# Optimization experiments

Hardware: AMD Instinct MI355X
Metric: run time of the kernel (lower is better)

The kernel has to match this reference:

```python
import jax, jax.numpy as jnp
import numpy as np


def setup_inputs() -> dict:
    key = jax.random.key(0)
    ks = jax.random.split(key, 7)
    B, N, D, F, E = 4, 2048, 1024, 4096, 8
    s_in = 1.0 / np.sqrt(D)
    s_ff = 1.0 / np.sqrt(F)
    return {
        "x": jax.random.normal(ks[0], (B, N, D), dtype=jnp.float32),
        "Wg": jax.random.normal(ks[1], (D, E), dtype=jnp.float32) * s_in,
        "bg": jnp.zeros((E,), dtype=jnp.float32),
        "W1": jax.random.normal(ks[2], (E, D, F), dtype=jnp.float32) * s_in,
        "b1": jnp.zeros((E, F), dtype=jnp.float32),
        "W2": jax.random.normal(ks[3], (E, F, D), dtype=jnp.float32) * s_ff,
        "b2": jnp.zeros((E, D), dtype=jnp.float32),
    }


def reference(x, Wg, bg, W1, b1, W2, b2):
    TOP_K = 2
    # Gating: softmax over experts, then top-k (dropout is inference no-op)
    gate_scores = jax.nn.softmax(x @ Wg + bg, axis=-1)          # [B,N,E]
    topk_scores, topk_idx = jax.lax.top_k(gate_scores, TOP_K)   # [B,N,K]

    # Dense all-expert FFN (matches reference: every expert on every token)
    h = jax.nn.relu(jnp.einsum("bnd,edf->ebnf", x, W1) + b1[:, None, None, :])
    eo = jnp.einsum("ebnf,efd->ebnd", h, W2) + b2[:, None, None, :]  # [E,B,N,D]

    # Gather top-k expert outputs per token and combine
    eo_bne = jnp.transpose(eo, (1, 2, 0, 3))                     # [B,N,E,D]
    gathered = jnp.take_along_axis(eo_bne, topk_idx[..., None], axis=2)  # [B,N,K,D]
    output = jnp.sum(topk_scores[..., None] * gathered, axis=2)  # [B,N,D]
    return output
```

## Files before the change

kernel.cpp:

```cpp
#include <hip/hip_runtime.h>
#include <stdint.h>


#define E_ 8
#define D_ 1024
#define F_ 4096
#define NTOK 8192

typedef __bf16 bf16x8 __attribute__((ext_vector_type(8)));
typedef float f32x4 __attribute__((ext_vector_type(4)));
typedef unsigned short ushort_t;

__device__ __forceinline__ ushort_t f2bf(float f) {
  union { float f; unsigned u; } v; v.f = f;
  unsigned r = v.u + 0x7fff + ((v.u >> 16) & 1);
  return (ushort_t)(r >> 16);
}

__device__ __forceinline__ void gload16(const void* g, void* l) {
  __builtin_amdgcn_global_load_lds((__attribute__((address_space(1))) void*)(g),
                                   (__attribute__((address_space(3))) void*)(l),
                                   16, 0, 0);
}

__global__ __launch_bounds__(256) void gate_k(const float* __restrict__ x,
    const float* __restrict__ Wg, const float* __restrict__ bg,
    int* counts, int* tk_idx, float* tk_score) {
  __shared__ float wg[D_ * E_];
  for (int i = threadIdx.x; i < D_ * E_; i += 256) wg[i] = Wg[i];
  __syncthreads();
  const int lane = threadIdx.x & 63;
  const int wv = threadIdx.x >> 6;
  const int t = blockIdx.x * 4 + wv;
  const float* xr = x + (size_t)t * D_;
  double acc[E_];
#pragma unroll
  for (int e = 0; e < E_; ++e) acc[e] = 0.0;
  for (int i = 0; i < D_ / 64; ++i) {
    const int d = i * 64 + lane;
    const double xv = (double)xr[d];
#pragma unroll
    for (int e = 0; e < E_; ++e) acc[e] += xv * (double)wg[d * E_ + e];
  }
#pragma unroll
  for (int e = 0; e < E_; ++e) {
    double v = acc[e];
#pragma unroll
    for (int s = 32; s > 0; s >>= 1) v += __shfl_xor(v, s, 64);
    acc[e] = v;
  }
  if (lane == 0) {
    double l[E_], m = -1e300;
#pragma unroll
    for (int e = 0; e < E_; ++e) { l[e] = acc[e] + (double)bg[e]; m = (l[e] > m) ? l[e] : m; }
    double p[E_], s = 0.0;
#pragma unroll
    for (int e = 0; e < E_; ++e) { p[e] = exp(l[e] - m); s += p[e]; }
    int i1 = 0;
#pragma unroll
    for (int e = 1; e < E_; ++e) if (p[e] > p[i1]) i1 = e;
    int i2 = -1;
#pragma unroll
    for (int e = 0; e < E_; ++e) if (e != i1 && (i2 < 0 || p[e] > p[i2])) i2 = e;
    tk_idx[2 * t] = i1; tk_idx[2 * t + 1] = i2;
    tk_score[2 * t] = (float)(p[i1] / s);
    tk_score[2 * t + 1] = (float)(p[i2] / s);
    atomicAdd(&counts[i1], 1);
    atomicAdd(&counts[i2], 1);
  }
}

__global__ void offsets_k(const int* __restrict__ counts, int* __restrict__ offsets) {
  if (threadIdx.x == 0) {
    int s = 0;
    for (int e = 0; e < E_; ++e) { offsets[e] = s; s += counts[e]; }
    offsets[E_] = s;
  }
}

__global__ __launch_bounds__(256) void assign_k(const int* __restrict__ tk_idx,
    const float* __restrict__ tk_score, const int* __restrict__ offsets,
    int* counts2, int* slot_token, float* slot_scale) {
  const int t = blockIdx.x * 256 + threadIdx.x;
#pragma unroll
  for (int k = 0; k < 2; ++k) {
    const int e = tk_idx[2 * t + k];
    const int pos = atomicAdd(&counts2[e], 1);
    const int slot = offsets[e] + pos;
    slot_token[slot] = t;
    slot_scale[slot] = tk_score[2 * t + k];
  }
}

__global__ __launch_bounds__(256) void convert_x_k(const float* __restrict__ x,
                                                   ushort_t* __restrict__ xb) {
  const size_t i = ((size_t)blockIdx.x * 256 + threadIdx.x) * 8;
  const float4 a = *(const float4*)(x + i);
  const float4 b = *(const float4*)(x + i + 4);
  union { ushort_t u[8]; uint4 v; } p;
  p.u[0] = f2bf(a.x); p.u[1] = f2bf(a.y); p.u[2] = f2bf(a.z); p.u[3] = f2bf(a.w);
  p.u[4] = f2bf(b.x); p.u[5] = f2bf(b.y); p.u[6] = f2bf(b.z); p.u[7] = f2bf(b.w);
  *(uint4*)(xb + i) = p.v;
}

__global__ __launch_bounds__(256) void transpose_conv(const float* __restrict__ in,
    ushort_t* __restrict__ out, int R, int C) {
  __shared__ float t[32][33];
  const int ex = blockIdx.z;
  const int r0 = blockIdx.y * 32, c0 = blockIdx.x * 32;
  const float* ein = in + (size_t)ex * R * C;
  ushort_t* eout = out + (size_t)ex * R * C;
  const int tx = threadIdx.x & 31, ty = threadIdx.x >> 5;
#pragma unroll
  for (int j = 0; j < 32; j += 8)
    t[ty + j][tx] = ein[(size_t)(r0 + ty + j) * C + (c0 + tx)];
  __syncthreads();
#pragma unroll
  for (int j = 0; j < 32; j += 8)
    eout[(size_t)(c0 + ty + j) * R + (r0 + tx)] = f2bf(t[tx][ty + j]);
}

template <int MODE>
__global__ __launch_bounds__(256) void moe_gemm(
    const ushort_t* __restrict__ A, const ushort_t* __restrict__ Bt,
    const float* __restrict__ bias,
    const int* __restrict__ offs, const int* __restrict__ counts,
    const int* __restrict__ slot_token, const float* __restrict__ slot_scale,
    ushort_t* __restrict__ H, float* __restrict__ Out, int N, int K) {
  const int e = blockIdx.z;
  const int cnt = counts[e];
  const int mb = blockIdx.y;
  if (mb * 128 >= cnt) return;
  const int off = offs[e];
  const int n0 = blockIdx.x * 128;

  __shared__ ushort_t As[128 * 32];
  __shared__ ushort_t Bs[128 * 32];

  const int lane = threadIdx.x & 63, wv = threadIdx.x >> 6;
  const int wm = wv >> 1, wn = wv & 1;
  const int sub = lane >> 2, quad = lane & 3;

  const ushort_t* ag[2];
  const ushort_t* bgp[2];
#pragma unroll
  for (int j = 0; j < 2; ++j) {
    const int row = j * 64 + wv * 16 + sub;
    int gm = mb * 128 + row;
    if (gm >= cnt) gm = cnt - 1;
    size_t arow;
    if (MODE == 0) arow = (size_t)slot_token[off + gm] * (size_t)K;
    else           arow = (size_t)(off + gm) * (size_t)K;
    ag[j] = A + arow + quad * 8;
    bgp[j] = Bt + ((size_t)e * N + (size_t)(n0 + row)) * (size_t)K + quad * 8;
  }
  ushort_t* al[2] = { As + (wv * 16) * 32, As + (64 + wv * 16) * 32 };
  ushort_t* bl[2] = { Bs + (wv * 16) * 32, Bs + (64 + wv * 16) * 32 };

  f32x4 acc[4][4];
#pragma unroll
  for (int i = 0; i < 4; ++i)
#pragma unroll
    for (int j = 0; j < 4; ++j) { acc[i][j][0] = 0.f; acc[i][j][1] = 0.f; acc[i][j][2] = 0.f; acc[i][j][3] = 0.f; }

  const int fr = lane & 15, kg = lane >> 4;
  const int nk = K / 32;
  for (int kt = 0; kt < nk; ++kt) {
    const int ko = kt * 32;
    gload16(ag[0] + ko, al[0]);
    gload16(ag[1] + ko, al[1]);
    gload16(bgp[0] + ko, bl[0]);
    gload16(bgp[1] + ko, bl[1]);
    __syncthreads();
    bf16x8 a[4], b[4];
#pragma unroll
    for (int i = 0; i < 4; ++i)
      a[i] = *(const bf16x8*)(As + (wm * 64 + i * 16 + fr) * 32 + kg * 8);
#pragma unroll
    for (int j = 0; j < 4; ++j)
      b[j] = *(const bf16x8*)(Bs + (wn * 64 + j * 16 + fr) * 32 + kg * 8);
#pragma unroll
    for (int i = 0; i < 4; ++i)
#pragma unroll
      for (int j = 0; j < 4; ++j)
        acc[i][j] = __builtin_amdgcn_mfma_f32_16x16x32_bf16(a[i], b[j], acc[i][j], 0, 0, 0);
    __syncthreads();
  }

  const int rg = lane >> 4;
#pragma unroll
  for (int i = 0; i < 4; ++i) {
#pragma unroll
    for (int q = 0; q < 4; ++q) {
      const int m = wm * 64 + i * 16 + rg * 4 + q;
      const int gm = mb * 128 + m;
      if (gm < cnt) {
        if (MODE == 0) {
          ushort_t* hr = H + (size_t)(off + gm) * (size_t)N + n0;
#pragma unroll
          for (int j = 0; j < 4; ++j) {
            const int n = wn * 64 + j * 16 + fr;
            float v = acc[i][j][q] + bias[(size_t)e * N + n0 + n];
            hr[n] = f2bf(v > 0.f ? v : 0.f);
          }
        } else {
          const int slot = off + gm;
          const int tok = slot_token[slot];
          const float sc = slot_scale[slot];
          float* orow = Out + (size_t)tok * D_ + n0;
#pragma unroll
          for (int j = 0; j < 4; ++j) {
            const int n = wn * 64 + j * 16 + fr;
            float v = acc[i][j][q] + bias[(size_t)e * N + n0 + n];
            atomicAdd(orow + n, sc * v);
          }
        }
      }
    }
  }
}

extern "C" void kernel_launch(void* const* d_in, const int* in_sizes, int n_in,
                              void* d_out, int out_size, void* d_ws, size_t ws_size,
                              hipStream_t stream) {
  const float* x  = (const float*)d_in[0];
  const float* Wg = (const float*)d_in[1];
  const float* bg = (const float*)d_in[2];
  const float* W1 = (const float*)d_in[3];
  const float* b1 = (const float*)d_in[4];
  const float* W2 = (const float*)d_in[5];
  const float* b2 = (const float*)d_in[6];
  float* out = (float*)d_out;
  char* ws = (char*)d_ws;

  int*   counts     = (int*)(ws + 0);
  int*   counts2    = (int*)(ws + 64);
  int*   offsets    = (int*)(ws + 128);
  int*   tk_idx     = (int*)(ws + 256);
  float* tk_score   = (float*)(ws + 256 + 65536);
  int*   slot_token = (int*)(ws + 256 + 2 * 65536);
  float* slot_scale = (float*)(ws + 256 + 3 * 65536);

  ushort_t* xb  = (ushort_t*)(ws + (1 << 20));
  ushort_t* w1t = xb + (size_t)NTOK * D_;
  ushort_t* w2t = w1t + (size_t)E_ * F_ * D_;
  ushort_t* h   = w2t + (size_t)E_ * D_ * F_;

  hipMemsetAsync(ws, 0, 256, stream);
  hipMemsetAsync(d_out, 0, sizeof(float) * (size_t)out_size, stream);

  convert_x_k<<<(NTOK * D_) / (256 * 8), 256, 0, stream>>>(x, xb);
  transpose_conv<<<dim3(F_ / 32, D_ / 32, E_), 256, 0, stream>>>(W1, w1t, D_, F_);
  transpose_conv<<<dim3(D_ / 32, F_ / 32, E_), 256, 0, stream>>>(W2, w2t, F_, D_);
  gate_k<<<NTOK / 4, 256, 0, stream>>>(x, Wg, bg, counts, tk_idx, tk_score);
  offsets_k<<<1, 64, 0, stream>>>(counts, offsets);
  assign_k<<<NTOK / 256, 256, 0, stream>>>(tk_idx, tk_score, offsets, counts2, slot_token, slot_scale);

  moe_gemm<0><<<dim3(F_ / 128, NTOK / 128, E_), 256, 0, stream>>>(
      xb, w1t, b1, offsets, counts, slot_token, slot_scale, h, nullptr, F_, D_);
  moe_gemm<1><<<dim3(D_ / 128, NTOK / 128, E_), 256, 0, stream>>>(
      h, w2t, b2, offsets, counts, slot_token, slot_scale, nullptr, out, D_, F_);
}
```

Measured before the change: 1.144 ms.

## Enlarge MoE GEMM tiles to 256x256 with double-buffered swizzled LDS

The grouped expert GEMM moves from 128x128 tiles with 256 threads and a K-step of 32 to 256x256 tiles with 512 threads and a K-step of 64. LDS is now double-buffered, so the next stage's global-to-LDS loads overlap the current MFMAs, and an XOR swizzle avoids LDS bank conflicts. The goal is more operand reuse per loaded byte and fewer barriers per unit of work. Separately, the weight transpose/convert kernel switches to 64x64 tiles with float4 reads and 16-byte bf16 writes, and the gate kernel stores Wg expert-major in LDS. The risks are register pressure from the 128 accumulator registers under launch_bounds(512,2), possible spills, and only one 128KB-LDS block fitting per CU.

```diff
diff --git a/kernel.cpp b/kernel.cpp
--- a/kernel.cpp
+++ b/kernel.cpp
@@ -26,8 +26,8 @@
 __global__ __launch_bounds__(256) void gate_k(const float* __restrict__ x,
     const float* __restrict__ Wg, const float* __restrict__ bg,
     int* counts, int* tk_idx, float* tk_score) {
-  __shared__ float wg[D_ * E_];
-  for (int i = threadIdx.x; i < D_ * E_; i += 256) wg[i] = Wg[i];
+  __shared__ float wg[E_ * D_];
+  for (int i = threadIdx.x; i < D_ * E_; i += 256) wg[(i & 7) * D_ + (i >> 3)] = Wg[i];
   __syncthreads();
   const int lane = threadIdx.x & 63;
   const int wv = threadIdx.x >> 6;
@@ -40,7 +40,7 @@
     const int d = i * 64 + lane;
     const double xv = (double)xr[d];
 #pragma unroll
-    for (int e = 0; e < E_; ++e) acc[e] += xv * (double)wg[d * E_ + e];
+    for (int e = 0; e < E_; ++e) acc[e] += xv * (double)wg[e * D_ + d];
   }
 #pragma unroll
   for (int e = 0; e < E_; ++e) {
@@ -105,23 +105,33 @@
 
 __global__ __launch_bounds__(256) void transpose_conv(const float* __restrict__ in,
     ushort_t* __restrict__ out, int R, int C) {
-  __shared__ float t[32][33];
+  __shared__ float t[64][65];
   const int ex = blockIdx.z;
-  const int r0 = blockIdx.y * 32, c0 = blockIdx.x * 32;
+  const int c0 = blockIdx.x * 64, r0 = blockIdx.y * 64;
   const float* ein = in + (size_t)ex * R * C;
   ushort_t* eout = out + (size_t)ex * R * C;
-  const int tx = threadIdx.x & 31, ty = threadIdx.x >> 5;
-#pragma unroll
-  for (int j = 0; j < 32; j += 8)
-    t[ty + j][tx] = ein[(size_t)(r0 + ty + j) * C + (c0 + tx)];
+  const int tid = threadIdx.x;
+#pragma unroll
+  for (int it = 0; it < 4; ++it) {
+    const int idx = it * 256 + tid;
+    const int r = idx >> 4, cv = (idx & 15) * 4;
+    const float4 v = *(const float4*)(ein + (size_t)(r0 + r) * C + c0 + cv);
+    t[cv + 0][r] = v.x; t[cv + 1][r] = v.y; t[cv + 2][r] = v.z; t[cv + 3][r] = v.w;
+  }
   __syncthreads();
 #pragma unroll
-  for (int j = 0; j < 32; j += 8)
-    eout[(size_t)(c0 + ty + j) * R + (r0 + tx)] = f2bf(t[tx][ty + j]);
+  for (int it = 0; it < 2; ++it) {
+    const int idx = it * 256 + tid;
+    const int c = idx >> 3, sg = (idx & 7) * 8;
+    union { ushort_t u[8]; uint4 v; } p;
+#pragma unroll
+    for (int k = 0; k < 8; ++k) p.u[k] = f2bf(t[c][sg + k]);
+    *(uint4*)(eout + (size_t)(c0 + c) * R + r0 + sg) = p.v;
+  }
 }
 
 template <int MODE>
-__global__ __launch_bounds__(256) void moe_gemm(
+__global__ __launch_bounds__(512, 2) void moe_gemm(
     const ushort_t* __restrict__ A, const ushort_t* __restrict__ Bt,
     const float* __restrict__ bias,
     const int* __restrict__ offs, const int* __restrict__ counts,
@@ -130,77 +140,97 @@
   const int e = blockIdx.z;
   const int cnt = counts[e];
   const int mb = blockIdx.y;
-  if (mb * 128 >= cnt) return;
+  if (mb * 256 >= cnt) return;
   const int off = offs[e];
-  const int n0 = blockIdx.x * 128;
-
-  __shared__ ushort_t As[128 * 32];
-  __shared__ ushort_t Bs[128 * 32];
-
-  const int lane = threadIdx.x & 63, wv = threadIdx.x >> 6;
-  const int wm = wv >> 1, wn = wv & 1;
-  const int sub = lane >> 2, quad = lane & 3;
-
-  const ushort_t* ag[2];
-  const ushort_t* bgp[2];
-#pragma unroll
-  for (int j = 0; j < 2; ++j) {
-    const int row = j * 64 + wv * 16 + sub;
-    int gm = mb * 128 + row;
+  const int n0 = blockIdx.x * 256;
+
+  extern __shared__ char smem[];
+
+  const int tid = threadIdx.x;
+  const int w = tid >> 6, l = tid & 63;
+  const int wm = w >> 2, wn = w & 3;
+
+  const int lr = l >> 3;
+  const int swk = ((l & 7) * 16) ^ (lr << 4);
+  const char* asrc[4];
+  const char* bsrc[4];
+#pragma unroll
+  for (int q = 0; q < 4; ++q) {
+    const int row = (w * 4 + q) * 8 + lr;
+    int gm = mb * 256 + row;
     if (gm >= cnt) gm = cnt - 1;
     size_t arow;
-    if (MODE == 0) arow = (size_t)slot_token[off + gm] * (size_t)K;
-    else           arow = (size_t)(off + gm) * (size_t)K;
-    ag[j] = A + arow + quad * 8;
-    bgp[j] = Bt + ((size_t)e * N + (size_t)(n0 + row)) * (size_t)K + quad * 8;
-  }
-  ushort_t* al[2] = { As + (wv * 16) * 32, As + (64 + wv * 16) * 32 };
-  ushort_t* bl[2] = { Bs + (wv * 16) * 32, Bs + (64 + wv * 16) * 32 };
-
-  f32x4 acc[4][4];
-#pragma unroll
-  for (int i = 0; i < 4; ++i)
+    if (MODE == 0) arow = (size_t)slot_token[off + gm];
+    else           arow = (size_t)(off + gm);
+    asrc[q] = (const char*)A + arow * (size_t)K * 2 + swk;
+    bsrc[q] = (const char*)Bt + ((size_t)e * N + (size_t)(n0 + row)) * (size_t)K * 2 + swk;
+  }
+
+  const int fr = l & 15, kg = l >> 4, rg = kg;
+  const int sw = (fr & 7) << 4;
+  const int baseA0 = (wm * 128 + fr) * 128 + ((kg * 16) ^ sw);
+  const int baseA1 = (wm * 128 + fr) * 128 + ((64 + kg * 16) ^ sw);
+  const int baseB0 = 32768 + (wn * 64 + fr) * 128 + ((kg * 16) ^ sw);
+  const int baseB1 = 32768 + (wn * 64 + fr) * 128 + ((64 + kg * 16) ^ sw);
+
+  f32x4 acc[8][4];
+#pragma unroll
+  for (int i = 0; i < 8; ++i)
 #pragma unroll
     for (int j = 0; j < 4; ++j) { acc[i][j][0] = 0.f; acc[i][j][1] = 0.f; acc[i][j][2] = 0.f; acc[i][j][3] = 0.f; }
 
-  const int fr = lane & 15, kg = lane >> 4;
-  const int nk = K / 32;
+  const int nk = K / 64;
+  int curOff = 0;
+
+#define STAGE(KOFF, LOFF)                                                     \
+  do {                                                                        \
+    _Pragma("unroll")                                                         \
+    for (int q = 0; q < 4; ++q)                                               \
+      gload16(asrc[q] + (KOFF), smem + (LOFF) + (w * 4 + q) * 1024);          \
+    _Pragma("unroll")                                                         \
+    for (int q = 0; q < 4; ++q)                                               \
+      gload16(bsrc[q] + (KOFF), smem + (LOFF) + 32768 + (w * 4 + q) * 1024);  \
+  } while (0)
+
+  STAGE(0, 0);
+  __syncthreads();
+
   for (int kt = 0; kt < nk; ++kt) {
-    const int ko = kt * 32;
-    gload16(ag[0] + ko, al[0]);
-    gload16(ag[1] + ko, al[1]);
-    gload16(bgp[0] + ko, bl[0]);
-    gload16(bgp[1] + ko, bl[1]);
+    if (kt + 1 < nk) STAGE((kt + 1) * 128, curOff ^ 65536);
+#pragma unroll
+    for (int s = 0; s < 2; ++s) {
+      bf16x8 a[8], b[4];
+      const int bA = curOff + (s ? baseA1 : baseA0);
+      const int bB = curOff + (s ? baseB1 : baseB0);
+#pragma unroll
+      for (int i = 0; i < 8; ++i) a[i] = *(const bf16x8*)(smem + bA + i * 2048);
+#pragma unroll
+      for (int j = 0; j < 4; ++j) b[j] = *(const bf16x8*)(smem + bB + j * 2048);
+#pragma unroll
+      for (int i = 0; i < 8; ++i)
+#pragma unroll
+        for (int j = 0; j < 4; ++j)
+          acc[i][j] = __builtin_amdgcn_mfma_f32_16x16x32_bf16(a[i], b[j], acc[i][j], 0, 0, 0);
+    }
     __syncthreads();
-    bf16x8 a[4], b[4];
-#pragma unroll
-    for (int i = 0; i < 4; ++i)
-      a[i] = *(const bf16x8*)(As + (wm * 64 + i * 16 + fr) * 32 + kg * 8);
-#pragma unroll
-    for (int j = 0; j < 4; ++j)
-      b[j] = *(const bf16x8*)(Bs + (wn * 64 + j * 16 + fr) * 32 + kg * 8);
-#pragma unroll
-    for (int i = 0; i < 4; ++i)
-#pragma unroll
-      for (int j = 0; j < 4; ++j)
-        acc[i][j] = __builtin_amdgcn_mfma_f32_16x16x32_bf16(a[i], b[j], acc[i][j], 0, 0, 0);
-    __syncthreads();
-  }
-
-  const int rg = lane >> 4;
-#pragma unroll
-  for (int i = 0; i < 4; ++i) {
+    curOff ^= 65536;
+  }
+#undef STAGE
+
+  const float* bias_e = bias + (size_t)e * N + n0;
+#pragma unroll
+  for (int i = 0; i < 8; ++i) {
 #pragma unroll
     for (int q = 0; q < 4; ++q) {
-      const int m = wm * 64 + i * 16 + rg * 4 + q;
-      const int gm = mb * 128 + m;
+      const int m = wm * 128 + i * 16 + rg * 4 + q;
+      const int gm = mb * 256 + m;
       if (gm < cnt) {
         if (MODE == 0) {
           ushort_t* hr = H + (size_t)(off + gm) * (size_t)N + n0;
 #pragma unroll
           for (int j = 0; j < 4; ++j) {
             const int n = wn * 64 + j * 16 + fr;
-            float v = acc[i][j][q] + bias[(size_t)e * N + n0 + n];
+            float v = acc[i][j][q] + bias_e[n];
             hr[n] = f2bf(v > 0.f ? v : 0.f);
           }
         } else {
@@ -211,7 +241,7 @@
 #pragma unroll
           for (int j = 0; j < 4; ++j) {
             const int n = wn * 64 + j * 16 + fr;
-            float v = acc[i][j][q] + bias[(size_t)e * N + n0 + n];
+            float v = acc[i][j][q] + bias_e[n];
             atomicAdd(orow + n, sc * v);
           }
         }
@@ -246,18 +276,23 @@
   ushort_t* w2t = w1t + (size_t)E_ * F_ * D_;
   ushort_t* h   = w2t + (size_t)E_ * D_ * F_;
 
+  (void)hipFuncSetAttribute((const void*)moe_gemm<0>,
+                            hipFuncAttributeMaxDynamicSharedMemorySize, 131072);
+  (void)hipFuncSetAttribute((const void*)moe_gemm<1>,
+                            hipFuncAttributeMaxDynamicSharedMemorySize, 131072);
+
   hipMemsetAsync(ws, 0, 256, stream);
   hipMemsetAsync(d_out, 0, sizeof(float) * (size_t)out_size, stream);
 
   convert_x_k<<<(NTOK * D_) / (256 * 8), 256, 0, stream>>>(x, xb);
-  transpose_conv<<<dim3(F_ / 32, D_ / 32, E_), 256, 0, stream>>>(W1, w1t, D_, F_);
-  transpose_conv<<<dim3(D_ / 32, F_ / 32, E_), 256, 0, stream>>>(W2, w2t, F_, D_);
+  transpose_conv<<<dim3(F_ / 64, D_ / 64, E_), 256, 0, stream>>>(W1, w1t, D_, F_);
+  transpose_conv<<<dim3(D_ / 64, F_ / 64, E_), 256, 0, stream>>>(W2, w2t, F_, D_);
   gate_k<<<NTOK / 4, 256, 0, stream>>>(x, Wg, bg, counts, tk_idx, tk_score);
   offsets_k<<<1, 64, 0, stream>>>(counts, offsets);
   assign_k<<<NTOK / 256, 256, 0, stream>>>(tk_idx, tk_score, offsets, counts2, slot_token, slot_scale);
 
-  moe_gemm<0><<<dim3(F_ / 128, NTOK / 128, E_), 256, 0, stream>>>(
+  moe_gemm<0><<<dim3(F_ / 256, 64, E_), 512, 131072, stream>>>(
       xb, w1t, b1, offsets, counts, slot_token, slot_scale, h, nullptr, F_, D_);
-  moe_gemm<1><<<dim3(D_ / 128, NTOK / 128, E_), 256, 0, stream>>>(
+  moe_gemm<1><<<dim3(D_ / 256, 64, E_), 512, 131072, stream>>>(
       h, w2t, b2, offsets, counts, slot_token, slot_scale, nullptr, out, D_, F_);
 }
```

Result: faster. 1.082 ms (-5.4%).
